# Optimization experiments

Measured on AMD Instinct MI355X. Metric: run time of the kernel, lower is better.

Reference implementation:

```python
import jax, jax.numpy as jnp
import numpy as np

B, G, F, U = 4, 4096, 256, 128
NEG = -1.0e9

def _glorot(key, shape):
    fan_in, fan_out = shape[0], shape[1]
    std = jnp.sqrt(2.0 / (fan_in + fan_out)).astype(jnp.float32)
    return jax.random.normal(key, shape, dtype=jnp.float32) * std

def setup_inputs() -> dict:
    key = jax.random.key(0)
    k = jax.random.split(key, 7)
    x = jax.random.normal(k[0], (B, G, F), dtype=jnp.float32)
    # binary adjacency (sparse-ish genomic graph), float32 as in the TF layer
    adj = (jax.random.uniform(k[1], (G, G)) < 0.02).astype(jnp.float32)
    adj = jnp.maximum(adj, jnp.eye(G, dtype=jnp.float32))  # keep self-edges
    return {
        "x": x,
        "adj": adj,
        "w": _glorot(k[2], (F, U)),
        "ai": _glorot(k[3], (U, G)),
        "aj": _glorot(k[4], (U, G)),
        "w_2": _glorot(k[5], (F, U)),
        "b_a": _glorot(k[6], (G, G)),
    }

def reference(x, adj, w, ai, aj, w_2, b_a):
    # f: [B, G, U]
    f = jnp.einsum("bgf,fu->bgu", x, w)
    self_attn = jnp.einsum("bgu,uh->bgh", f, ai)            # [B, G, G]
    other_attn = jnp.einsum("bgu,uh->bhg", f, aj)           # transpose of f@aj
    attn = self_attn + other_attn + NEG * (1.0 - adj) + b_a
    gate_h = jax.nn.sigmoid(attn)                             # [B, G, G]
    # (f^T @ gate_h)^T  ->  out[b,h,u] = sum_g f[b,g,u] * gate_h[b,g,h]
    agg = jnp.einsum("bgu,bgh->bhu", f, gate_h)             # [B, G, U]
    out = jax.nn.relu(agg + jnp.einsum("bgf,fu->bgu", x, w_2))
    return out, gate_h
```

## Files before the change

kernel.cpp:

```cpp
#include <hip/hip_runtime.h>
#include <hip/hip_bf16.h>

#define B_ 4
#define G_ 4096
#define F_ 256
#define U_ 128

typedef __bf16 v8bf __attribute__((ext_vector_type(8)));
typedef float f32x4 __attribute__((ext_vector_type(4)));

__device__ __forceinline__ unsigned short f2bf(float x) {
    union { float f; unsigned u; } v; v.f = x;
    unsigned r = v.u + 0x7FFFu + ((v.u >> 16) & 1u);
    return (unsigned short)(r >> 16);
}
__device__ __forceinline__ float bf2f(unsigned short s) {
    union { unsigned u; float f; } v; v.u = ((unsigned)s) << 16; return v.f;
}

typedef const __attribute__((address_space(1))) unsigned int* gas_t;
typedef __attribute__((address_space(3))) unsigned int* las_t;

__device__ __forceinline__ void gld16(const void* g, const void* l) {
    __builtin_amdgcn_global_load_lds((gas_t)(unsigned long long)g,
                                     (las_t)(unsigned)(unsigned long long)l, 16, 0, 0);
}

#define WAITV(n) asm volatile("s_waitcnt vmcnt(" #n ")" ::: "memory")
#define LGKM0    asm volatile("s_waitcnt lgkmcnt(0)" ::: "memory")
#define SBAR     __builtin_amdgcn_s_barrier()
#define SCHED0   __builtin_amdgcn_sched_barrier(0)


#define OFF_FG   0
#define OFF_AJ   24576
#define OFF_BA   49152
#define OFF_GT   73728
#define LDS_SZ   81920

__global__ __launch_bounds__(256) void k_transpose_w(
    const float* __restrict__ w, const float* __restrict__ w2,
    unsigned short* __restrict__ wT, unsigned short* __restrict__ w2T)
{
    int bx = blockIdx.x;
    const float* src = (bx & 1) ? w2 : w;
    unsigned short* dst = (bx & 1) ? w2T : wT;
    int u = threadIdx.x & 127;
    int kseg = (threadIdx.x >> 7) + (bx >> 1) * 2;
    #pragma unroll
    for (int k = 0; k < 16; ++k) {
        int kk = kseg * 16 + k;
        dst[(size_t)u * F_ + kk] = f2bf(src[(size_t)kk * U_ + u]);
    }
}

__global__ __launch_bounds__(256) void k_transpose_aiaj(
    const float* __restrict__ ai, const float* __restrict__ aj,
    unsigned short* __restrict__ Ai, unsigned short* __restrict__ Aj)
{
    __shared__ unsigned short s_t[64 * 128];
    int blk = blockIdx.x;
    const float* src = (blk < 64) ? ai : aj;
    unsigned short* dst = (blk < 64) ? Ai : Aj;
    int gtile = (blk & 63) * 64;
    int tid = threadIdx.x;
    int gl = tid & 63, ub = tid >> 6;
    #pragma unroll
    for (int i = 0; i < 32; ++i) {
        int u = ub * 32 + i;
        float v = src[(size_t)u * G_ + gtile + gl];
        int ad = ((gl << 8) + (u << 1)) ^ ((gl & 7) << 4);
        *(unsigned short*)((char*)s_t + ad) = f2bf(v);
    }
    __syncthreads();
    int c = tid >> 4, sub = tid & 15;
    int g4l = c >> 2, k5 = c & 3;
    #pragma unroll
    for (int q = 0; q < 4; ++q) {
        int l = sub * 4 + q;
        int g = g4l * 16 + (l & 15);
        int u = k5 * 32 + (l >> 4) * 8;
        uint4 v = *(const uint4*)((const char*)s_t + (g << 8) + ((u << 1) ^ ((g & 7) << 4)));
        *(uint4*)(dst + (((size_t)((gtile >> 4) + g4l) * 4 + k5) * 64 + l) * 8) = v;
    }
}

__global__ __launch_bounds__(256) void k_bias16(
    const float* __restrict__ adj, const float* __restrict__ ba,
    unsigned short* __restrict__ ct)
{
    size_t i = ((size_t)blockIdx.x * 256 + threadIdx.x) * 8;
    float4 a0 = *(const float4*)(adj + i);
    float4 a1 = *(const float4*)(adj + i + 4);
    float4 b0 = *(const float4*)(ba + i);
    float4 b1 = *(const float4*)(ba + i + 4);
    union { unsigned short s[8]; uint4 v; } o;
    o.s[0] = f2bf(fmaf(a0.x, 1e9f, -1e9f) + b0.x);
    o.s[1] = f2bf(fmaf(a0.y, 1e9f, -1e9f) + b0.y);
    o.s[2] = f2bf(fmaf(a0.z, 1e9f, -1e9f) + b0.z);
    o.s[3] = f2bf(fmaf(a0.w, 1e9f, -1e9f) + b0.w);
    o.s[4] = f2bf(fmaf(a1.x, 1e9f, -1e9f) + b1.x);
    o.s[5] = f2bf(fmaf(a1.y, 1e9f, -1e9f) + b1.y);
    o.s[6] = f2bf(fmaf(a1.z, 1e9f, -1e9f) + b1.z);
    o.s[7] = f2bf(fmaf(a1.w, 1e9f, -1e9f) + b1.w);
    *(uint4*)(ct + i) = o.v;
}

__global__ __launch_bounds__(256, 2) void k_gemm_f(
    const float* __restrict__ x,
    const unsigned short* __restrict__ wT, const unsigned short* __restrict__ w2T,
    unsigned short* __restrict__ Ff, unsigned short* __restrict__ FfT,
    float* __restrict__ g2_out)
{
    __shared__ unsigned short s_xa[128 * 128];
    __shared__ unsigned short s_w[128 * 128];
    __shared__ unsigned short s_w2[128 * 128];
    const int tid = threadIdx.x;
    const int lane = tid & 63, w = tid >> 6;
    const int l15 = lane & 15, l4 = lane >> 4;
    const int wm = w >> 1, wn = w & 1;
    const int mrow0 = blockIdx.x * 128;

    f32x4 zz = {0.f, 0.f, 0.f, 0.f};
    f32x4 accf[4][4], accg[4][4];
    #pragma unroll
    for (int i = 0; i < 4; ++i)
        #pragma unroll
        for (int j = 0; j < 4; ++j) { accf[i][j] = zz; accg[i][j] = zz; }

    for (int kc = 0; kc < 2; ++kc) {
        if (kc) __syncthreads();
        {
            int m = tid >> 1, half = tid & 1;
            const float* src = x + (size_t)(mrow0 + m) * F_ + kc * 128 + half * 64;
            unsigned tmp32[32];
            #pragma unroll
            for (int i = 0; i < 16; ++i) {
                float4 v = *(const float4*)(src + i * 4);
                tmp32[i * 2 + 0] = (unsigned)f2bf(v.x) | ((unsigned)f2bf(v.y) << 16);
                tmp32[i * 2 + 1] = (unsigned)f2bf(v.z) | ((unsigned)f2bf(v.w) << 16);
            }
            #pragma unroll
            for (int gi2 = 0; gi2 < 8; ++gi2) {
                int ad = (m << 8) + ((half * 128 + gi2 * 16) ^ ((m & 7) << 4));
                *(uint4*)((char*)s_xa + ad) = *(const uint4*)(tmp32 + gi2 * 4);
            }
        }
        #pragma unroll
        for (int i = 0; i < 8; ++i) {
            int c = w * 8 + i;
            int row = c * 4 + l4;
            int Wp = (l15 << 4) ^ ((row & 7) << 4);
            gld16((const char*)wT  + (size_t)row * 512 + kc * 256 + Wp, (const char*)s_w  + c * 1024);
            gld16((const char*)w2T + (size_t)row * 512 + kc * 256 + Wp, (const char*)s_w2 + c * 1024);
        }
        __syncthreads();
        #pragma unroll
        for (int ks = 0; ks < 4; ++ks) {
            int kb = 64 * ks + 16 * l4;
            v8bf a[4], b1[4], b2[4];
            #pragma unroll
            for (int mf = 0; mf < 4; ++mf) {
                int m = l15 + 16 * mf + 64 * wm;
                int ad = (m << 8) + (kb ^ ((m & 7) << 4));
                a[mf] = *(const v8bf*)((const char*)s_xa + ad);
            }
            #pragma unroll
            for (int nf = 0; nf < 4; ++nf) {
                int u = l15 + 16 * nf + 64 * wn;
                int ad = (u << 8) + (kb ^ ((u & 7) << 4));
                b1[nf] = *(const v8bf*)((const char*)s_w + ad);
                b2[nf] = *(const v8bf*)((const char*)s_w2 + ad);
            }
            #pragma unroll
            for (int mf = 0; mf < 4; ++mf)
                #pragma unroll
                for (int nf = 0; nf < 4; ++nf) {
                    accf[mf][nf] = __builtin_amdgcn_mfma_f32_16x16x32_bf16(a[mf], b1[nf], accf[mf][nf], 0, 0, 0);
                    accg[mf][nf] = __builtin_amdgcn_mfma_f32_16x16x32_bf16(a[mf], b2[nf], accg[mf][nf], 0, 0, 0);
                }
        }
    }
    const int b = mrow0 >> 12, gb = mrow0 & 4095;
    #pragma unroll
    for (int mf = 0; mf < 4; ++mf)
        #pragma unroll
        for (int nf = 0; nf < 4; ++nf)
            #pragma unroll
            for (int r = 0; r < 4; ++r) {
                int m = 4 * l4 + r + 16 * mf + 64 * wm;
                int u = l15 + 16 * nf + 64 * wn;
                g2_out[(size_t)(mrow0 + m) * U_ + u] = accg[mf][nf][r];
            }
    __syncthreads();
    #pragma unroll
    for (int mf = 0; mf < 4; ++mf)
        #pragma unroll
        for (int nf = 0; nf < 4; ++nf)
            #pragma unroll
            for (int r = 0; r < 4; ++r) {
                int m = 4 * l4 + r + 16 * mf + 64 * wm;
                int u = l15 + 16 * nf + 64 * wn;
                int ad = (m << 8) + ((u << 1) ^ ((m & 7) << 4));
                *(unsigned short*)((char*)s_xa + ad) = f2bf(accf[mf][nf][r]);
            }
    __syncthreads();
    {
        unsigned short* Ffb = Ff + (size_t)b * (G_ * U_);
        int c = tid >> 3, sub = tid & 7;
        int g4l = c >> 2, k5 = c & 3;
        #pragma unroll
        for (int q = 0; q < 8; ++q) {
            int l = sub * 8 + q;
            int m = g4l * 16 + (l & 15);
            int k = k5 * 32 + (l >> 4) * 8;
            uint4 v = *(const uint4*)((const char*)s_xa + (m << 8) + ((k << 1) ^ ((m & 7) << 4)));
            *(uint4*)(Ffb + (((size_t)((gb >> 4) + g4l) * 4 + k5) * 64 + l) * 8) = v;
        }
    }
    {
        unsigned short* FfTb = FfT + (size_t)b * (G_ * U_);
        int c = tid >> 3, sub = tid & 7;
        int u4 = c >> 2, g5l = c & 3;
        #pragma unroll
        for (int q = 0; q < 8; ++q) {
            int l = sub * 8 + q;
            int u = u4 * 16 + (l & 15);
            int g0l = g5l * 32 + (l >> 4) * 8;
            union { unsigned short s[8]; uint4 v; } pk;
            #pragma unroll
            for (int j = 0; j < 8; ++j) {
                int m = g0l + j;
                pk.s[j] = *(const unsigned short*)((const char*)s_xa + (m << 8) + ((u << 1) ^ ((m & 7) << 4)));
            }
            *(uint4*)(FfTb + (((size_t)u4 * 128 + (gb >> 5) + g5l) * 64 + l) * 8) = pk.v;
        }
    }
}

__device__ __forceinline__ void stage_all(const unsigned short* Ff_b, const unsigned short* Aj,
                                          const unsigned short* ct, char* smem,
                                          int w, int lane, int gt, int htile, int slot)
{
    #pragma unroll
    for (int i = 0; i < 2; ++i) {
        int c = 2 * w + i;
        size_t off = ((((size_t)(gt >> 4) + (c >> 2)) * 4 + (c & 3)) * 64 + lane) * 16;
        gld16((const char*)Ff_b + off, smem + OFF_FG + slot * 8192 + c * 1024);
        gld16((const char*)Aj  + off, smem + OFF_AJ + slot * 8192 + c * 1024);
        int row = 4 * c + (lane >> 4);
        int src = ((lane & 15) * 16) ^ ((row & 7) << 4);
        gld16((const char*)ct + ((size_t)(gt + row) * G_ + htile) * 2 + src,
              smem + OFF_BA + slot * 8192 + c * 1024);
    }
}

__global__ __launch_bounds__(256, 2) void k_main(
    const unsigned short* __restrict__ Ff,
    const unsigned short* __restrict__ FfT,
    const unsigned short* __restrict__ Ai,
    const unsigned short* __restrict__ Aj,
    const unsigned short* __restrict__ ct16,
    float* __restrict__ gate_out,
    float* __restrict__ part)
{
    __shared__ __align__(1024) char smem[LDS_SZ];
    const int tid = threadIdx.x;
    const int lane = tid & 63, w = tid >> 6;
    const int l15 = lane & 15, l4 = lane >> 4;
    const int bid = blockIdx.x;
    const int xcd = bid & 7;
    const int rest = bid >> 3;
    const int b = rest & 3;
    const int tile = (rest >> 2) * 8 + xcd;
    const int split = tile & 3;
    const int htile = (tile >> 2) * 128;

    const unsigned short* Ff_b  = Ff  + (size_t)b * (G_ * U_);
    const unsigned short* FfT_b = FfT + (size_t)b * (G_ * U_);
    float* gate_b = gate_out + ((size_t)b << 24);

    #pragma unroll
    for (int i = 0; i < 8; ++i) {
        int c = 8 * w + i;
        size_t off = ((((size_t)(htile >> 4) + (c >> 2)) * 4 + (c & 3)) * 64 + lane) * 16;
        gld16((const char*)Ai + off, smem + c * 1024);
    }
    WAITV(0); SBAR;
    v8bf aih[2][4], fh[2][4];
    #pragma unroll
    for (int hf = 0; hf < 2; ++hf)
        #pragma unroll
        for (int ks = 0; ks < 4; ++ks)
            aih[hf][ks] = *(const v8bf*)(smem + (8 * w + 4 * hf + ks) * 1024 + lane * 16);
    LGKM0; SBAR;
    #pragma unroll
    for (int i = 0; i < 8; ++i) {
        int c = 8 * w + i;
        size_t off = ((((size_t)(htile >> 4) + (c >> 2)) * 4 + (c & 3)) * 64 + lane) * 16;
        gld16((const char*)Ff_b + off, smem + c * 1024);
    }
    WAITV(0); SBAR;
    #pragma unroll
    for (int hf = 0; hf < 2; ++hf)
        #pragma unroll
        for (int ks = 0; ks < 4; ++ks)
            fh[hf][ks] = *(const v8bf*)(smem + (8 * w + 4 * hf + ks) * 1024 + lane * 16);
    LGKM0; SBAR;
    stage_all(Ff_b, Aj, ct16, smem, w, lane, split * 1024, htile, 0);
    stage_all(Ff_b, Aj, ct16, smem, w, lane, split * 1024 + 32, htile, 1);
    WAITV(6);

    f32x4 zz = {0.f, 0.f, 0.f, 0.f};
    f32x4 agga[2][8];
    #pragma unroll
    for (int i = 0; i < 2; ++i)
        #pragma unroll
        for (int j = 0; j < 8; ++j) agga[i][j] = zz;

    int sl = 0;
    for (int it = 0; it < 32; ++it) {
        const int gtile = split * 1024 + it * 32;
        const int itn = (it < 30) ? it + 2 : 31;
        const int gnext = split * 1024 + itn * 32;
        int sl2 = sl + 2; if (sl2 >= 3) sl2 -= 3;

        v8bf ft[8];
        #pragma unroll
        for (int u4 = 0; u4 < 8; ++u4)
            ft[u4] = *(const v8bf*)(FfT_b + (((size_t)u4 * 128 + (gtile >> 5)) * 64 + lane) * 8);

        stage_all(Ff_b, Aj, ct16, smem, w, lane, gnext, htile, sl2);

        WAITV(32); LGKM0; SBAR; SCHED0;

        f32x4 acc[2][2];
        #pragma unroll
        for (int i = 0; i < 2; ++i)
            #pragma unroll
            for (int j = 0; j < 2; ++j) acc[i][j] = zz;
        {
            const char* bfg = smem + OFF_FG + sl * 8192;
            const char* baj = smem + OFF_AJ + sl * 8192;
            #pragma unroll
            for (int ks = 0; ks < 4; ++ks) {
                v8bf fgv[2], ajv[2];
                #pragma unroll
                for (int gf = 0; gf < 2; ++gf) {
                    fgv[gf] = *(const v8bf*)(bfg + (gf * 4 + ks) * 1024 + lane * 16);
                    ajv[gf] = *(const v8bf*)(baj + (gf * 4 + ks) * 1024 + lane * 16);
                }
                #pragma unroll
                for (int hf = 0; hf < 2; ++hf)
                    #pragma unroll
                    for (int gf = 0; gf < 2; ++gf) {
                        acc[hf][gf] = __builtin_amdgcn_mfma_f32_16x16x32_bf16(aih[hf][ks], fgv[gf], acc[hf][gf], 0, 0, 0);
                        acc[hf][gf] = __builtin_amdgcn_mfma_f32_16x16x32_bf16(fh[hf][ks],  ajv[gf], acc[hf][gf], 0, 0, 0);
                    }
            }
        }

        #pragma unroll
        for (int gf = 0; gf < 2; ++gf)
            #pragma unroll
            for (int hf = 0; hf < 2; ++hf) {
                int g = 16 * gf + l15;
                int h0 = 32 * w + 16 * hf + 4 * l4;
                ushort4 bu = *(const ushort4*)(smem + OFF_BA + sl * 8192 + g * 256 +
                                               ((h0 * 2) ^ ((g & 7) << 4)));
                f32x4 gs;
                #pragma unroll
                for (int r = 0; r < 4; ++r) {
                    float attnv = acc[hf][gf][r] + bf2f((&bu.x)[r]);
                    float e = __expf(-attnv);
                    float gv = __builtin_amdgcn_rcpf(1.0f + e);
                    gs[r] = gv;
                    int hL = h0 + r;
                    *(unsigned short*)(smem + OFF_GT + hL * 64 +
                                       ((g * 2) ^ (((hL >> 2) & 3) << 4))) = f2bf(gv);
                }
                __builtin_nontemporal_store(gs,
                    (f32x4*)(gate_b + (size_t)(gtile + g) * G_ + htile + h0));
            }

        LGKM0; SBAR; SCHED0;

        {
            v8bf ag[2];
            #pragma unroll
            for (int hf = 0; hf < 2; ++hf) {
                int hr = 32 * w + 16 * hf + l15;
                ag[hf] = *(const v8bf*)(smem + OFF_GT + hr * 64 +
                                        ((l4 * 16) ^ (((hr >> 2) & 3) << 4)));
            }
            #pragma unroll
            for (int hf = 0; hf < 2; ++hf)
                #pragma unroll
                for (int u4 = 0; u4 < 8; ++u4)
                    agga[hf][u4] = __builtin_amdgcn_mfma_f32_16x16x32_bf16(ag[hf], ft[u4], agga[hf][u4], 0, 0, 0);
        }

        sl = (sl + 1 == 3) ? 0 : sl + 1;
    }

    #pragma unroll
    for (int hf = 0; hf < 2; ++hf)
        #pragma unroll
        for (int u4 = 0; u4 < 8; ++u4)
            #pragma unroll
            for (int r = 0; r < 4; ++r) {
                int h = htile + 32 * w + 16 * hf + 4 * l4 + r;
                int u = 16 * u4 + l15;
                part[(((size_t)b * 4 + split) << 19) + (size_t)h * U_ + u] = agga[hf][u4][r];
            }
}

__global__ __launch_bounds__(256) void k_reduce(const float4* __restrict__ part, float4* __restrict__ outio)
{
    int i = blockIdx.x * 256 + threadIdx.x;
    int fb = i >> 17, r = i & 0x1FFFF;
    const float4* p = part + (((size_t)fb * 4) << 17) + r;
    float4 p0 = p[0];
    float4 p1 = p[(size_t)1 << 17];
    float4 p2 = p[(size_t)2 << 17];
    float4 p3 = p[(size_t)3 << 17];
    float4 g = outio[i];
    float4 o;
    o.x = fmaxf(p0.x + p1.x + p2.x + p3.x + g.x, 0.f);
    o.y = fmaxf(p0.y + p1.y + p2.y + p3.y + g.y, 0.f);
    o.z = fmaxf(p0.z + p1.z + p2.z + p3.z + g.z, 0.f);
    o.w = fmaxf(p0.w + p1.w + p2.w + p3.w + g.w, 0.f);
    outio[i] = o;
}

extern "C" void kernel_launch(void* const* d_in, const int* in_sizes, int n_in,
                              void* d_out, int out_size, void* d_ws, size_t ws_size,
                              hipStream_t stream)
{
    (void)in_sizes; (void)n_in; (void)out_size; (void)ws_size;
    const float* x   = (const float*)d_in[0];
    const float* adj = (const float*)d_in[1];
    const float* w   = (const float*)d_in[2];
    const float* ai  = (const float*)d_in[3];
    const float* aj  = (const float*)d_in[4];
    const float* w2  = (const float*)d_in[5];
    const float* ba  = (const float*)d_in[6];

    char* ws = (char*)d_ws;
    unsigned short* Ff  = (unsigned short*)(ws);
    unsigned short* FfT = (unsigned short*)(ws + ((size_t)4 << 20));
    unsigned short* Ai  = (unsigned short*)(ws + ((size_t)8 << 20));
    unsigned short* Aj  = (unsigned short*)(ws + ((size_t)9 << 20));
    unsigned short* wT  = (unsigned short*)(ws + ((size_t)10 << 20));
    unsigned short* w2T = (unsigned short*)(ws + ((size_t)10 << 20) + (1 << 17));
    float* part         = (float*)(ws + ((size_t)12 << 20));
    unsigned short* ct16= (unsigned short*)(ws + ((size_t)44 << 20));

    float* out  = (float*)d_out;
    float* gate = out + (size_t)B_ * G_ * U_;

    k_transpose_w   <<<dim3(16),   dim3(256), 0, stream>>>(w, w2, wT, w2T);
    k_transpose_aiaj<<<dim3(128),  dim3(256), 0, stream>>>(ai, aj, Ai, Aj);
    k_bias16        <<<dim3(8192), dim3(256), 0, stream>>>(adj, ba, ct16);
    k_gemm_f        <<<dim3(128),  dim3(256), 0, stream>>>(x, wT, w2T, Ff, FfT, out);
    k_main          <<<dim3(512),  dim3(256), 0, stream>>>(Ff, FfT, Ai, Aj, ct16, gate, part);
    k_reduce        <<<dim3(2048), dim3(256), 0, stream>>>((const float4*)part, (float4*)out);
}
```

Measured before the change: 158.4 us.

## Merge prep kernels and software-pipeline FfT loads with reordered barriers in main loop

Fuses the three preprocessing kernels (bias, ai/aj transpose, w transpose) into one launch selected by block index, removing two kernel launches. In the main loop, the barrier and wait now come first, the next stage is issued after the barrier, and the FfT register tile for the following iteration is prefetched one iteration ahead. The barrier before the aggregation MFMA is dropped, and the MFMA sections are wrapped in s_setprio. Dropping that barrier relies on the top-of-loop barrier to order the gate tile in LDS between waves. The extra prefetch registers may raise register pressure.

```diff
diff --git a/kernel.cpp b/kernel.cpp
--- a/kernel.cpp
+++ b/kernel.cpp
@@ -38,72 +38,69 @@
 #define OFF_GT   73728
 #define LDS_SZ   81920
 
-__global__ __launch_bounds__(256) void k_transpose_w(
+__global__ __launch_bounds__(256) void k_prep(
+    const float* __restrict__ adj, const float* __restrict__ ba,
+    unsigned short* __restrict__ ct,
+    const float* __restrict__ ai, const float* __restrict__ aj,
+    unsigned short* __restrict__ Ai, unsigned short* __restrict__ Aj,
     const float* __restrict__ w, const float* __restrict__ w2,
     unsigned short* __restrict__ wT, unsigned short* __restrict__ w2T)
 {
-    int bx = blockIdx.x;
-    const float* src = (bx & 1) ? w2 : w;
-    unsigned short* dst = (bx & 1) ? w2T : wT;
-    int u = threadIdx.x & 127;
-    int kseg = (threadIdx.x >> 7) + (bx >> 1) * 2;
-    #pragma unroll
-    for (int k = 0; k < 16; ++k) {
-        int kk = kseg * 16 + k;
-        dst[(size_t)u * F_ + kk] = f2bf(src[(size_t)kk * U_ + u]);
-    }
-}
-
-__global__ __launch_bounds__(256) void k_transpose_aiaj(
-    const float* __restrict__ ai, const float* __restrict__ aj,
-    unsigned short* __restrict__ Ai, unsigned short* __restrict__ Aj)
-{
     __shared__ unsigned short s_t[64 * 128];
-    int blk = blockIdx.x;
-    const float* src = (blk < 64) ? ai : aj;
-    unsigned short* dst = (blk < 64) ? Ai : Aj;
-    int gtile = (blk & 63) * 64;
-    int tid = threadIdx.x;
-    int gl = tid & 63, ub = tid >> 6;
-    #pragma unroll
-    for (int i = 0; i < 32; ++i) {
-        int u = ub * 32 + i;
-        float v = src[(size_t)u * G_ + gtile + gl];
-        int ad = ((gl << 8) + (u << 1)) ^ ((gl & 7) << 4);
-        *(unsigned short*)((char*)s_t + ad) = f2bf(v);
-    }
-    __syncthreads();
-    int c = tid >> 4, sub = tid & 15;
-    int g4l = c >> 2, k5 = c & 3;
-    #pragma unroll
-    for (int q = 0; q < 4; ++q) {
-        int l = sub * 4 + q;
-        int g = g4l * 16 + (l & 15);
-        int u = k5 * 32 + (l >> 4) * 8;
-        uint4 v = *(const uint4*)((const char*)s_t + (g << 8) + ((u << 1) ^ ((g & 7) << 4)));
-        *(uint4*)(dst + (((size_t)((gtile >> 4) + g4l) * 4 + k5) * 64 + l) * 8) = v;
-    }
-}
-
-__global__ __launch_bounds__(256) void k_bias16(
-    const float* __restrict__ adj, const float* __restrict__ ba,
-    unsigned short* __restrict__ ct)
-{
-    size_t i = ((size_t)blockIdx.x * 256 + threadIdx.x) * 8;
-    float4 a0 = *(const float4*)(adj + i);
-    float4 a1 = *(const float4*)(adj + i + 4);
-    float4 b0 = *(const float4*)(ba + i);
-    float4 b1 = *(const float4*)(ba + i + 4);
-    union { unsigned short s[8]; uint4 v; } o;
-    o.s[0] = f2bf(fmaf(a0.x, 1e9f, -1e9f) + b0.x);
-    o.s[1] = f2bf(fmaf(a0.y, 1e9f, -1e9f) + b0.y);
-    o.s[2] = f2bf(fmaf(a0.z, 1e9f, -1e9f) + b0.z);
-    o.s[3] = f2bf(fmaf(a0.w, 1e9f, -1e9f) + b0.w);
-    o.s[4] = f2bf(fmaf(a1.x, 1e9f, -1e9f) + b1.x);
-    o.s[5] = f2bf(fmaf(a1.y, 1e9f, -1e9f) + b1.y);
-    o.s[6] = f2bf(fmaf(a1.z, 1e9f, -1e9f) + b1.z);
-    o.s[7] = f2bf(fmaf(a1.w, 1e9f, -1e9f) + b1.w);
-    *(uint4*)(ct + i) = o.v;
+    const int bid = blockIdx.x;
+    const int tid = threadIdx.x;
+    if (bid < 8192) {
+        size_t i = ((size_t)bid * 256 + tid) * 8;
+        float4 a0 = *(const float4*)(adj + i);
+        float4 a1 = *(const float4*)(adj + i + 4);
+        float4 b0 = *(const float4*)(ba + i);
+        float4 b1 = *(const float4*)(ba + i + 4);
+        union { unsigned short s[8]; uint4 v; } o;
+        o.s[0] = f2bf(fmaf(a0.x, 1e9f, -1e9f) + b0.x);
+        o.s[1] = f2bf(fmaf(a0.y, 1e9f, -1e9f) + b0.y);
+        o.s[2] = f2bf(fmaf(a0.z, 1e9f, -1e9f) + b0.z);
+        o.s[3] = f2bf(fmaf(a0.w, 1e9f, -1e9f) + b0.w);
+        o.s[4] = f2bf(fmaf(a1.x, 1e9f, -1e9f) + b1.x);
+        o.s[5] = f2bf(fmaf(a1.y, 1e9f, -1e9f) + b1.y);
+        o.s[6] = f2bf(fmaf(a1.z, 1e9f, -1e9f) + b1.z);
+        o.s[7] = f2bf(fmaf(a1.w, 1e9f, -1e9f) + b1.w);
+        *(uint4*)(ct + i) = o.v;
+    } else if (bid < 8320) {
+        int blk = bid - 8192;
+        const float* src = (blk < 64) ? ai : aj;
+        unsigned short* dst = (blk < 64) ? Ai : Aj;
+        int gtile = (blk & 63) * 64;
+        int gl = tid & 63, ub = tid >> 6;
+        #pragma unroll
+        for (int i = 0; i < 32; ++i) {
+            int u = ub * 32 + i;
+            float v = src[(size_t)u * G_ + gtile + gl];
+            int ad = ((gl << 8) + (u << 1)) ^ ((gl & 7) << 4);
+            *(unsigned short*)((char*)s_t + ad) = f2bf(v);
+        }
+        __syncthreads();
+        int c = tid >> 4, sub = tid & 15;
+        int g4l = c >> 2, k5 = c & 3;
+        #pragma unroll
+        for (int q = 0; q < 4; ++q) {
+            int l = sub * 4 + q;
+            int g = g4l * 16 + (l & 15);
+            int u = k5 * 32 + (l >> 4) * 8;
+            uint4 v = *(const uint4*)((const char*)s_t + (g << 8) + ((u << 1) ^ ((g & 7) << 4)));
+            *(uint4*)(dst + (((size_t)((gtile >> 4) + g4l) * 4 + k5) * 64 + l) * 8) = v;
+        }
+    } else {
+        int bx = bid - 8320;
+        const float* src = (bx & 1) ? w2 : w;
+        unsigned short* dst = (bx & 1) ? w2T : wT;
+        int u = tid & 127;
+        int kseg = (tid >> 7) + (bx >> 1) * 2;
+        #pragma unroll
+        for (int k = 0; k < 16; ++k) {
+            int kk = kseg * 16 + k;
+            dst[(size_t)u * F_ + kk] = f2bf(src[(size_t)kk * U_ + u]);
+        }
+    }
 }
 
 __global__ __launch_bounds__(256, 2) void k_gemm_f(
@@ -309,7 +306,11 @@
     LGKM0; SBAR;
     stage_all(Ff_b, Aj, ct16, smem, w, lane, split * 1024, htile, 0);
     stage_all(Ff_b, Aj, ct16, smem, w, lane, split * 1024 + 32, htile, 1);
-    WAITV(6);
+    v8bf ft[8];
+    #pragma unroll
+    for (int u4 = 0; u4 < 8; ++u4)
+        ft[u4] = *(const v8bf*)(FfT_b + (((size_t)u4 * 128 + ((split * 1024) >> 5)) * 64 + lane) * 8);
+    WAITV(0); SBAR;
 
     f32x4 zz = {0.f, 0.f, 0.f, 0.f};
     f32x4 agga[2][8];
@@ -321,18 +322,21 @@
     int sl = 0;
     for (int it = 0; it < 32; ++it) {
         const int gtile = split * 1024 + it * 32;
-        const int itn = (it < 30) ? it + 2 : 31;
-        const int gnext = split * 1024 + itn * 32;
+        const int it2 = (it < 30) ? it + 2 : 31;
+        const int g2t = split * 1024 + it2 * 32;
+        const int it1 = (it < 31) ? it + 1 : 31;
+        const int g1t = split * 1024 + it1 * 32;
         int sl2 = sl + 2; if (sl2 >= 3) sl2 -= 3;
 
-        v8bf ft[8];
+        WAITV(30); LGKM0; SBAR; SCHED0;
+
+        stage_all(Ff_b, Aj, ct16, smem, w, lane, g2t, htile, sl2);
+        SCHED0;
+        v8bf ftn[8];
         #pragma unroll
         for (int u4 = 0; u4 < 8; ++u4)
-            ft[u4] = *(const v8bf*)(FfT_b + (((size_t)u4 * 128 + (gtile >> 5)) * 64 + lane) * 8);
-
-        stage_all(Ff_b, Aj, ct16, smem, w, lane, gnext, htile, sl2);
-
-        WAITV(32); LGKM0; SBAR; SCHED0;
+            ftn[u4] = *(const v8bf*)(FfT_b + (((size_t)u4 * 128 + (g1t >> 5)) * 64 + lane) * 8);
+        SCHED0;
 
         f32x4 acc[2][2];
         #pragma unroll
@@ -342,6 +346,7 @@
         {
             const char* bfg = smem + OFF_FG + sl * 8192;
             const char* baj = smem + OFF_AJ + sl * 8192;
+            __builtin_amdgcn_s_setprio(1);
             #pragma unroll
             for (int ks = 0; ks < 4; ++ks) {
                 v8bf fgv[2], ajv[2];
@@ -358,6 +363,7 @@
                         acc[hf][gf] = __builtin_amdgcn_mfma_f32_16x16x32_bf16(fh[hf][ks],  ajv[gf], acc[hf][gf], 0, 0, 0);
                     }
             }
+            __builtin_amdgcn_s_setprio(0);
         }
 
         #pragma unroll
@@ -383,7 +389,7 @@
                     (f32x4*)(gate_b + (size_t)(gtile + g) * G_ + htile + h0));
             }
 
-        LGKM0; SBAR; SCHED0;
+        LGKM0; SCHED0;
 
         {
             v8bf ag[2];
@@ -393,12 +399,16 @@
                 ag[hf] = *(const v8bf*)(smem + OFF_GT + hr * 64 +
                                         ((l4 * 16) ^ (((hr >> 2) & 3) << 4)));
             }
+            __builtin_amdgcn_s_setprio(1);
             #pragma unroll
             for (int hf = 0; hf < 2; ++hf)
                 #pragma unroll
                 for (int u4 = 0; u4 < 8; ++u4)
                     agga[hf][u4] = __builtin_amdgcn_mfma_f32_16x16x32_bf16(ag[hf], ft[u4], agga[hf][u4], 0, 0, 0);
-        }
+            __builtin_amdgcn_s_setprio(0);
+        }
+        #pragma unroll
+        for (int u4 = 0; u4 < 8; ++u4) ft[u4] = ftn[u4];
 
         sl = (sl + 1 == 3) ? 0 : sl + 1;
     }
@@ -459,10 +469,8 @@
     float* out  = (float*)d_out;
     float* gate = out + (size_t)B_ * G_ * U_;
 
-    k_transpose_w   <<<dim3(16),   dim3(256), 0, stream>>>(w, w2, wT, w2T);
-    k_transpose_aiaj<<<dim3(128),  dim3(256), 0, stream>>>(ai, aj, Ai, Aj);
-    k_bias16        <<<dim3(8192), dim3(256), 0, stream>>>(adj, ba, ct16);
-    k_gemm_f        <<<dim3(128),  dim3(256), 0, stream>>>(x, wT, w2T, Ff, FfT, out);
-    k_main          <<<dim3(512),  dim3(256), 0, stream>>>(Ff, FfT, Ai, Aj, ct16, gate, part);
-    k_reduce        <<<dim3(2048), dim3(256), 0, stream>>>((const float4*)part, (float4*)out);
-}
+    k_prep   <<<dim3(8336), dim3(256), 0, stream>>>(adj, ba, ct16, ai, aj, Ai, Aj, w, w2, wT, w2T);
+    k_gemm_f <<<dim3(128),  dim3(256), 0, stream>>>(x, wT, w2T, Ff, FfT, out);
+    k_main   <<<dim3(512),  dim3(256), 0, stream>>>(Ff, FfT, Ai, Aj, ct16, gate, part);
+    k_reduce <<<dim3(2048), dim3(256), 0, stream>>>((const float4*)part, (float4*)out);
+}
```

Result: slower. 189.0 us (+19.3%).
